# Kernel tuning notes

Measured on AMD Instinct MI355X. Metric: run time of the kernel, lower is better.

Reference implementation:

```python
import jax, jax.numpy as jnp
import numpy as np

B, T, C, H = 4, 4096, 1024, 128

def setup_inputs() -> dict:
    key = jax.random.key(0)
    k1, k2, k3, k4 = jax.random.split(key, 4)
    ix = jax.random.normal(k1, (B, T, C), dtype=jnp.float32)
    Wq = jax.random.normal(k2, (C, H), dtype=jnp.float32) * (C ** -0.5)
    Wk = jax.random.normal(k3, (C, H), dtype=jnp.float32) * (C ** -0.5)
    Wv = jax.random.normal(k4, (C, H), dtype=jnp.float32) * (C ** -0.5)
    return {"ix": ix, "Wq": Wq, "Wk": Wk, "Wv": Wv}

def reference(ix, Wq, Wk, Wv):
    Bc, Tc, Cc = ix.shape
    q = ix @ Wq                      # [B,T,H]
    k = ix @ Wk                      # [B,T,H]
    v = ix @ Wv                      # [B,T,H]
    # NOTE: original computes k @ q^T (row index from k, col index from q),
    # scaled by n_embed**-0.5 (C, not head_size).
    wei = jnp.einsum('bth,bsh->bts', k, q) * (Cc ** -0.5)  # [B,T,T]
    causal = jnp.tril(jnp.ones((Tc, Tc), dtype=bool))
    wei = jnp.where(causal[None, :, :], wei, -jnp.inf)
    wei = jax.nn.softmax(wei, axis=-1)
    # dropout is identity in eval mode
    out = jnp.einsum('bts,bsh->bth', wei, v)  # [B,T,H]
    return out
```

## Files before the change

kernel.cpp:

```cpp
#include <hip/hip_runtime.h>
#include <hip/hip_bf16.h>

typedef __bf16 bf16x8 __attribute__((ext_vector_type(8)));
typedef float f32x4 __attribute__((ext_vector_type(4)));
#define MFMA16 __builtin_amdgcn_mfma_f32_16x16x32_bf16

static constexpr int Bsz = 4, T = 4096, C = 1024, H = 128;
static constexpr int BT = Bsz * T;

__device__ __forceinline__ void gl2lds16(const __bf16* g, __bf16* l) {
    __builtin_amdgcn_global_load_lds(
        (const __attribute__((address_space(1))) void*)g,
        (__attribute__((address_space(3))) void*)l, 16, 0, 0);
}

__global__ __launch_bounds__(256) void k_wprep(
    const float* __restrict__ Wq, const float* __restrict__ Wk,
    const float* __restrict__ Wv, __bf16* __restrict__ WTall)
{
    int idx = blockIdx.x * 256 + threadIdx.x;
    int n = idx >> 10, k = idx & 1023;
    int mat = n >> 7, col = n & 127;
    const float* W = mat == 0 ? Wq : (mat == 1 ? Wk : Wv);
    float s = (mat == 1) ? 0.045084220f : 1.0f;
    WTall[idx] = (__bf16)(W[k * H + col] * s);
}

__global__ __launch_bounds__(512) void k_proj(
    const float* __restrict__ X, const __bf16* __restrict__ WTall,
    __bf16* __restrict__ Qp, __bf16* __restrict__ Kp, __bf16* __restrict__ VT)
{
    union Smem {
        struct { __bf16 a[2][64 * 64]; __bf16 b[2][192 * 64]; } s;
        __bf16 vt_e[128][72];
    };
    __shared__ Smem su;

    const int tid = threadIdx.x;
    const int lane = tid & 63, w = tid >> 6;
    const int c = lane & 15, hi = lane >> 4;
    const int wm = w >> 2, wn = w & 3;
    const int ny = blockIdx.x & 1;
    const int m0 = (blockIdx.x >> 1) * 64;
    const int xorv = (c & 7) << 3;

    const int arow = tid >> 3, ac8 = tid & 7;
    const float* aSrc = X + (size_t)(m0 + arow) * C + ac8 * 8;
    const int aDst = arow * 64 + ((ac8 * 8) ^ ((arow & 7) << 3));
    const int brl = lane >> 3, bch = lane & 7;
    const __bf16* Wbase = WTall + (size_t)ny * 192 * 1024;

    f32x4 acc[2][3];
    #pragma unroll
    for (int i = 0; i < 2; ++i)
        #pragma unroll
        for (int j = 0; j < 3; ++j) acc[i][j] = (f32x4){0.f, 0.f, 0.f, 0.f};

    #pragma unroll
    for (int ib = 0; ib < 3; ++ib) {
        int row = w * 24 + ib * 8 + brl;
        int ch = bch ^ (row & 7);
        gl2lds16(Wbase + (size_t)row * 1024 + ch * 8, &su.s.b[0][(w * 3 + ib) * 512]);
    }
    {
        float4 f0 = *(const float4*)aSrc;
        float4 f1 = *(const float4*)(aSrc + 4);
        bf16x8 av;
        av[0] = (__bf16)f0.x; av[1] = (__bf16)f0.y; av[2] = (__bf16)f0.z; av[3] = (__bf16)f0.w;
        av[4] = (__bf16)f1.x; av[5] = (__bf16)f1.y; av[6] = (__bf16)f1.z; av[7] = (__bf16)f1.w;
        *(bf16x8*)&su.s.a[0][aDst] = av;
    }
    __syncthreads();

    for (int t = 0; t < 16; ++t) {
        int cur = t & 1;
        float4 g0, g1;
        if (t < 15) {
            int k0 = (t + 1) * 64;
            #pragma unroll
            for (int ib = 0; ib < 3; ++ib) {
                int row = w * 24 + ib * 8 + brl;
                int ch = bch ^ (row & 7);
                gl2lds16(Wbase + (size_t)row * 1024 + k0 + ch * 8,
                         &su.s.b[cur ^ 1][(w * 3 + ib) * 512]);
            }
            g0 = *(const float4*)(aSrc + k0);
            g1 = *(const float4*)(aSrc + k0 + 4);
        }
        #pragma unroll
        for (int kk = 0; kk < 2; ++kk) {
            bf16x8 a0 = *(const bf16x8*)&su.s.a[cur][(wm * 32 + c) * 64 + ((kk * 32 + hi * 8) ^ xorv)];
            bf16x8 a1 = *(const bf16x8*)&su.s.a[cur][(wm * 32 + 16 + c) * 64 + ((kk * 32 + hi * 8) ^ xorv)];
            #pragma unroll
            for (int fn = 0; fn < 3; ++fn) {
                bf16x8 bb = *(const bf16x8*)&su.s.b[cur][(wn * 48 + fn * 16 + c) * 64 + ((kk * 32 + hi * 8) ^ xorv)];
                acc[0][fn] = MFMA16(a0, bb, acc[0][fn], 0, 0, 0);
                acc[1][fn] = MFMA16(a1, bb, acc[1][fn], 0, 0, 0);
            }
        }
        if (t < 15) {
            bf16x8 av;
            av[0] = (__bf16)g0.x; av[1] = (__bf16)g0.y; av[2] = (__bf16)g0.z; av[3] = (__bf16)g0.w;
            av[4] = (__bf16)g1.x; av[5] = (__bf16)g1.y; av[6] = (__bf16)g1.z; av[7] = (__bf16)g1.w;
            *(bf16x8*)&su.s.a[cur ^ 1][aDst] = av;
        }
        __syncthreads();
    }

    #pragma unroll
    for (int mi = 0; mi < 2; ++mi) {
        int rowl = wm * 32 + mi * 16 + hi * 4;
        #pragma unroll
        for (int fn = 0; fn < 3; ++fn) {
            int nb = ny * 192 + wn * 48 + fn * 16;
            int mat = nb >> 7, colb = (nb & 127) + c;
            #pragma unroll
            for (int r = 0; r < 4; ++r) {
                __bf16 v = (__bf16)acc[mi][fn][r];
                if (mat == 0)      Qp[(size_t)(m0 + rowl + r) * H + colb] = v;
                else if (mat == 1) Kp[(size_t)(m0 + rowl + r) * H + colb] = v;
                else               su.vt_e[colb][rowl + r] = v;
            }
        }
    }
    __syncthreads();
    if (ny == 1) {
        int d = tid >> 2, tc = (tid & 3) * 16;
        int b = m0 >> 12, tl = m0 & (T - 1);
        __bf16* dst = VT + ((size_t)b * H + d) * T + tl + tc;
        const __bf16* s2 = &su.vt_e[d][tc];
        *(uint4*)dst = *(const uint4*)s2;
        *(uint4*)(dst + 8) = *(const uint4*)(s2 + 8);
    }
}

__global__ __launch_bounds__(256) void k_attn(
    const __bf16* __restrict__ Ka, const __bf16* __restrict__ Qb,
    const __bf16* __restrict__ VT, float* __restrict__ Out,
    float* __restrict__ Po, float* __restrict__ Pl)
{
    __shared__ __bf16 pl[4][32][40];
    __shared__ float oacc[64][132];
    __shared__ float sml[4][32];

    const int tid = threadIdx.x, lane = tid & 63, w = tid >> 6;
    const int c = lane & 15, hi = lane >> 4;
    const int wm = w >> 1, ws = w & 1;

    const int bi = blockIdx.x;
    const int p = bi & 1, b = (bi >> 1) & 3, u = bi >> 3;

    const __bf16* Kb  = Ka + (size_t)b * T * H;
    const __bf16* Qbb = Qb + (size_t)b * T * H;
    const __bf16* Vb  = VT + (size_t)b * H * T;

    bf16x8 ones;
    #pragma unroll
    for (int q8 = 0; q8 < 8; ++q8) ones[q8] = (__bf16)1.0f;

    #pragma unroll 1
    for (int half = 0; half < 2; ++half) {
        const int j  = half ? (63 - u) : u;
        const int t0 = j * 64;
        const int nsteps = j + 1;
        const int rbase = t0 + wm * 32;

        bf16x8 af[2][4];
        #pragma unroll
        for (int mi = 0; mi < 2; ++mi)
            #pragma unroll
            for (int kc = 0; kc < 4; ++kc)
                af[mi][kc] = *(const bf16x8*)(Kb + (size_t)(rbase + mi * 16 + c) * H + kc * 32 + hi * 8);

        f32x4 o[2][8], ol[2];
        #pragma unroll
        for (int mi = 0; mi < 2; ++mi) {
            #pragma unroll
            for (int nt = 0; nt < 8; ++nt) o[mi][nt] = (f32x4){0.f, 0.f, 0.f, 0.f};
            ol[mi] = (f32x4){0.f, 0.f, 0.f, 0.f};
        }

        for (int i = p; i < nsteps; i += 2) {
            const int sbase = i * 64 + ws * 32;
            f32x4 sa[2][2];
            sa[0][0] = (f32x4){0.f, 0.f, 0.f, 0.f}; sa[0][1] = sa[0][0];
            sa[1][0] = sa[0][0]; sa[1][1] = sa[0][0];
            #pragma unroll
            for (int sc = 0; sc < 2; ++sc) {
                bf16x8 bq[4];
                #pragma unroll
                for (int kc = 0; kc < 4; ++kc)
                    bq[kc] = *(const bf16x8*)(Qbb + (size_t)(sbase + sc * 16 + c) * H + kc * 32 + hi * 8);
                #pragma unroll
                for (int kc = 0; kc < 4; ++kc) {
                    sa[0][sc] = MFMA16(af[0][kc], bq[kc], sa[0][sc], 0, 0, 0);
                    sa[1][sc] = MFMA16(af[1][kc], bq[kc], sa[1][sc], 0, 0, 0);
                }
            }
            const bool dz = (sbase + 31 > rbase);
            #pragma unroll
            for (int mi = 0; mi < 2; ++mi)
                #pragma unroll
                for (int sc = 0; sc < 2; ++sc)
                    #pragma unroll
                    for (int r = 0; r < 4; ++r) {
                        float e = __builtin_amdgcn_exp2f(sa[mi][sc][r]);
                        if (dz) {
                            int tg = rbase + mi * 16 + hi * 4 + r;
                            if (sbase + sc * 16 + c > tg) e = 0.f;
                        }
                        pl[w][mi * 16 + hi * 4 + r][sc * 16 + c] = (__bf16)e;
                    }
            #pragma unroll
            for (int mi = 0; mi < 2; ++mi) {
                bf16x8 pf = *(const bf16x8*)&pl[w][mi * 16 + c][hi * 8];
                ol[mi] = MFMA16(pf, ones, ol[mi], 0, 0, 0);
                #pragma unroll
                for (int nt = 0; nt < 8; ++nt) {
                    bf16x8 vb = *(const bf16x8*)(Vb + (size_t)(nt * 16 + c) * T + sbase + hi * 8);
                    o[mi][nt] = MFMA16(pf, vb, o[mi][nt], 0, 0, 0);
                }
            }
        }

        if (c == 0) {
            #pragma unroll
            for (int mi = 0; mi < 2; ++mi)
                #pragma unroll
                for (int r = 0; r < 4; ++r)
                    sml[w][mi * 16 + hi * 4 + r] = ol[mi][r];
        }
        if (ws == 0) {
            #pragma unroll
            for (int mi = 0; mi < 2; ++mi)
                #pragma unroll
                for (int nt = 0; nt < 8; ++nt)
                    #pragma unroll
                    for (int r = 0; r < 4; ++r)
                        oacc[wm * 32 + mi * 16 + hi * 4 + r][nt * 16 + c] = o[mi][nt][r];
        }
        __syncthreads();
        if (ws == 1) {
            #pragma unroll
            for (int mi = 0; mi < 2; ++mi)
                #pragma unroll
                for (int nt = 0; nt < 8; ++nt)
                    #pragma unroll
                    for (int r = 0; r < 4; ++r)
                        oacc[wm * 32 + mi * 16 + hi * 4 + r][nt * 16 + c] += o[mi][nt][r];
        }
        __syncthreads();
        {
            int row = tid >> 2, cq = (tid & 3) * 4;
            float L = sml[(row >> 5) * 2][row & 31] + sml[(row >> 5) * 2 + 1][row & 31];
            float* dst = (p == 0 ? Out : Po) + ((size_t)b * T + t0 + row) * H;
            #pragma unroll
            for (int k = 0; k < 8; ++k) {
                int col = cq + k * 16;
                float4 v;
                v.x = oacc[row][col];
                v.y = oacc[row][col + 1];
                v.z = oacc[row][col + 2];
                v.w = oacc[row][col + 3];
                *(float4*)(dst + col) = v;
            }
            if ((tid & 3) == 0) Pl[(size_t)p * BT + b * T + t0 + row] = L;
        }
        __syncthreads();
    }
}

__global__ __launch_bounds__(256) void k_merge(
    float* __restrict__ Out, const float* __restrict__ Po,
    const float* __restrict__ Pl)
{
    size_t idx = ((size_t)blockIdx.x * 256 + threadIdx.x) * 8;
    size_t row = idx >> 7;
    float inv = 1.0f / (Pl[row] + Pl[BT + row]);
    float4 a0 = *(const float4*)(Out + idx);
    float4 a1 = *(const float4*)(Out + idx + 4);
    float4 p0 = *(const float4*)(Po + idx);
    float4 p1 = *(const float4*)(Po + idx + 4);
    float4 r0, r1;
    r0.x = (a0.x + p0.x) * inv; r0.y = (a0.y + p0.y) * inv;
    r0.z = (a0.z + p0.z) * inv; r0.w = (a0.w + p0.w) * inv;
    r1.x = (a1.x + p1.x) * inv; r1.y = (a1.y + p1.y) * inv;
    r1.z = (a1.z + p1.z) * inv; r1.w = (a1.w + p1.w) * inv;
    *(float4*)(Out + idx)     = r0;
    *(float4*)(Out + idx + 4) = r1;
}

extern "C" void kernel_launch(void* const* d_in, const int* in_sizes, int n_in,
                              void* d_out, int out_size, void* d_ws, size_t ws_size,
                              hipStream_t stream) {
    const float* ix = (const float*)d_in[0];
    const float* Wq = (const float*)d_in[1];
    const float* Wk = (const float*)d_in[2];
    const float* Wv = (const float*)d_in[3];
    float* out = (float*)d_out;

    __bf16* WTall = (__bf16*)d_ws;
    __bf16* Qp = WTall + 393216;
    __bf16* Kp = Qp + (size_t)BT * H;
    __bf16* VT = Kp + (size_t)BT * H;
    float*  Po = (float*)(VT + (size_t)BT * H);
    float*  Pl = Po + (size_t)BT * H;

    k_wprep<<<dim3(1536), 256, 0, stream>>>(Wq, Wk, Wv, WTall);
    k_proj<<<dim3(512), 512, 0, stream>>>(ix, WTall, Qp, Kp, VT);
    k_attn<<<dim3(256), 256, 0, stream>>>(Kp, Qp, VT, out, Po, Pl);
    k_merge<<<dim3(1024), 256, 0, stream>>>(out, Po, Pl);
}
```

Measured before the change: 110.3 us.

## Split attention key loop across 16 waves per block with LDS reduction

The attention kernel grows from 4 to 16 waves per block. The extra waves split the causal key steps four ways inside each block, and their partial output and row-sum accumulators are combined in shared memory over 8 serialized passes separated by barriers. The goal is to raise occupancy and latency hiding, since each CU previously ran only 4 waves. The P·V inner loop is also reordered so each V fragment is loaded once and reused for both row tiles. The cost is extra reduction passes and barriers, plus a 1024-thread launch bound that caps per-wave registers and may cause spills.

```diff
diff --git a/kernel.cpp b/kernel.cpp
--- a/kernel.cpp
+++ b/kernel.cpp
@@ -134,18 +134,18 @@
     }
 }
 
-__global__ __launch_bounds__(256) void k_attn(
+__global__ __launch_bounds__(1024) void k_attn(
     const __bf16* __restrict__ Ka, const __bf16* __restrict__ Qb,
     const __bf16* __restrict__ VT, float* __restrict__ Out,
     float* __restrict__ Po, float* __restrict__ Pl)
 {
-    __shared__ __bf16 pl[4][32][40];
+    __shared__ __bf16 pl[16][32][40];
     __shared__ float oacc[64][132];
-    __shared__ float sml[4][32];
+    __shared__ float sml[16][32];
 
     const int tid = threadIdx.x, lane = tid & 63, w = tid >> 6;
     const int c = lane & 15, hi = lane >> 4;
-    const int wm = w >> 1, ws = w & 1;
+    const int wm = (w >> 3) & 1, ws = (w >> 2) & 1, sp = w & 3;
 
     const int bi = blockIdx.x;
     const int p = bi & 1, b = (bi >> 1) & 3, u = bi >> 3;
@@ -180,7 +180,7 @@
             ol[mi] = (f32x4){0.f, 0.f, 0.f, 0.f};
         }
 
-        for (int i = p; i < nsteps; i += 2) {
+        for (int i = p + 2 * sp; i < nsteps; i += 8) {
             const int sbase = i * 64 + ws * 32;
             f32x4 sa[2][2];
             sa[0][0] = (f32x4){0.f, 0.f, 0.f, 0.f}; sa[0][1] = sa[0][0];
@@ -211,15 +211,15 @@
                         }
                         pl[w][mi * 16 + hi * 4 + r][sc * 16 + c] = (__bf16)e;
                     }
-            #pragma unroll
-            for (int mi = 0; mi < 2; ++mi) {
-                bf16x8 pf = *(const bf16x8*)&pl[w][mi * 16 + c][hi * 8];
-                ol[mi] = MFMA16(pf, ones, ol[mi], 0, 0, 0);
-                #pragma unroll
-                for (int nt = 0; nt < 8; ++nt) {
-                    bf16x8 vb = *(const bf16x8*)(Vb + (size_t)(nt * 16 + c) * T + sbase + hi * 8);
-                    o[mi][nt] = MFMA16(pf, vb, o[mi][nt], 0, 0, 0);
-                }
+            bf16x8 pf0 = *(const bf16x8*)&pl[w][c][hi * 8];
+            bf16x8 pf1 = *(const bf16x8*)&pl[w][16 + c][hi * 8];
+            ol[0] = MFMA16(pf0, ones, ol[0], 0, 0, 0);
+            ol[1] = MFMA16(pf1, ones, ol[1], 0, 0, 0);
+            #pragma unroll
+            for (int nt = 0; nt < 8; ++nt) {
+                bf16x8 vb = *(const bf16x8*)(Vb + (size_t)(nt * 16 + c) * T + sbase + hi * 8);
+                o[0][nt] = MFMA16(pf0, vb, o[0][nt], 0, 0, 0);
+                o[1][nt] = MFMA16(pf1, vb, o[1][nt], 0, 0, 0);
             }
         }
 
@@ -230,41 +230,36 @@
                 for (int r = 0; r < 4; ++r)
                     sml[w][mi * 16 + hi * 4 + r] = ol[mi][r];
         }
-        if (ws == 0) {
-            #pragma unroll
-            for (int mi = 0; mi < 2; ++mi)
-                #pragma unroll
-                for (int nt = 0; nt < 8; ++nt)
+        __syncthreads();
+        for (int g = 0; g < 8; ++g) {
+            if ((w & 7) == g) {
+                #pragma unroll
+                for (int mi = 0; mi < 2; ++mi)
                     #pragma unroll
-                    for (int r = 0; r < 4; ++r)
-                        oacc[wm * 32 + mi * 16 + hi * 4 + r][nt * 16 + c] = o[mi][nt][r];
-        }
-        __syncthreads();
-        if (ws == 1) {
-            #pragma unroll
-            for (int mi = 0; mi < 2; ++mi)
-                #pragma unroll
-                for (int nt = 0; nt < 8; ++nt)
-                    #pragma unroll
-                    for (int r = 0; r < 4; ++r)
-                        oacc[wm * 32 + mi * 16 + hi * 4 + r][nt * 16 + c] += o[mi][nt][r];
-        }
-        __syncthreads();
+                    for (int nt = 0; nt < 8; ++nt)
+                        #pragma unroll
+                        for (int r = 0; r < 4; ++r) {
+                            int row = wm * 32 + mi * 16 + hi * 4 + r, col = nt * 16 + c;
+                            if (g == 0) oacc[row][col]  = o[mi][nt][r];
+                            else        oacc[row][col] += o[mi][nt][r];
+                        }
+            }
+            __syncthreads();
+        }
         {
-            int row = tid >> 2, cq = (tid & 3) * 4;
-            float L = sml[(row >> 5) * 2][row & 31] + sml[(row >> 5) * 2 + 1][row & 31];
-            float* dst = (p == 0 ? Out : Po) + ((size_t)b * T + t0 + row) * H;
-            #pragma unroll
-            for (int k = 0; k < 8; ++k) {
-                int col = cq + k * 16;
-                float4 v;
-                v.x = oacc[row][col];
-                v.y = oacc[row][col + 1];
-                v.z = oacc[row][col + 2];
-                v.w = oacc[row][col + 3];
-                *(float4*)(dst + col) = v;
-            }
-            if ((tid & 3) == 0) Pl[(size_t)p * BT + b * T + t0 + row] = L;
+            int row = tid >> 4, col0 = (tid & 15) * 8;
+            float L = 0.f;
+            #pragma unroll
+            for (int g = 0; g < 8; ++g) L += sml[(row >> 5) * 8 + g][row & 31];
+            float* dst = (p == 0 ? Out : Po) + ((size_t)b * T + t0 + row) * H + col0;
+            float4 v0, v1;
+            v0.x = oacc[row][col0];     v0.y = oacc[row][col0 + 1];
+            v0.z = oacc[row][col0 + 2]; v0.w = oacc[row][col0 + 3];
+            v1.x = oacc[row][col0 + 4]; v1.y = oacc[row][col0 + 5];
+            v1.z = oacc[row][col0 + 6]; v1.w = oacc[row][col0 + 7];
+            *(float4*)dst       = v0;
+            *(float4*)(dst + 4) = v1;
+            if ((tid & 15) == 0) Pl[(size_t)p * BT + b * T + t0 + row] = L;
         }
         __syncthreads();
     }
@@ -308,6 +303,6 @@
 
     k_wprep<<<dim3(1536), 256, 0, stream>>>(Wq, Wk, Wv, WTall);
     k_proj<<<dim3(512), 512, 0, stream>>>(ix, WTall, Qp, Kp, VT);
-    k_attn<<<dim3(256), 256, 0, stream>>>(Kp, Qp, VT, out, Po, Pl);
+    k_attn<<<dim3(256), 1024, 0, stream>>>(Kp, Qp, VT, out, Po, Pl);
     k_merge<<<dim3(1024), 256, 0, stream>>>(out, Po, Pl);
 }
```

Measured after the change: 155.5 us. 1.41x slower.

## Software-pipeline Q/V register loads in attention loop and remap projection block indices

Applied to the files above, without the earlier changes.

The attention inner loop now double-buffers the Q and V fragments in registers, issuing global loads for the next step before computing the current one so memory latency overlaps the MFMA and exp work. The MFMAs are also interleaved across independent accumulators. Separately, the projection kernel's block index mapping changes so consecutive blocks cover different row tiles of the same weight half instead of alternating halves. Keeping a second set of fragments live raises register pressure and can reduce occupancy. The diagonal mask condition also changes from > to >=, which is harmless.

```diff
diff --git a/kernel.cpp b/kernel.cpp
--- a/kernel.cpp
+++ b/kernel.cpp
@@ -40,8 +40,8 @@
     const int lane = tid & 63, w = tid >> 6;
     const int c = lane & 15, hi = lane >> 4;
     const int wm = w >> 2, wn = w & 3;
-    const int ny = blockIdx.x & 1;
-    const int m0 = (blockIdx.x >> 1) * 64;
+    const int ny = blockIdx.x >> 8;
+    const int m0 = (blockIdx.x & 255) * 64;
     const int xorv = (c & 7) << 3;
 
     const int arow = tid >> 3, ac8 = tid & 7;
@@ -180,48 +180,71 @@
             ol[mi] = (f32x4){0.f, 0.f, 0.f, 0.f};
         }
 
-        for (int i = p; i < nsteps; i += 2) {
-            const int sbase = i * 64 + ws * 32;
-            f32x4 sa[2][2];
-            sa[0][0] = (f32x4){0.f, 0.f, 0.f, 0.f}; sa[0][1] = sa[0][0];
-            sa[1][0] = sa[0][0]; sa[1][1] = sa[0][0];
-            #pragma unroll
-            for (int sc = 0; sc < 2; ++sc) {
-                bf16x8 bq[4];
-                #pragma unroll
-                for (int kc = 0; kc < 4; ++kc)
-                    bq[kc] = *(const bf16x8*)(Qbb + (size_t)(sbase + sc * 16 + c) * H + kc * 32 + hi * 8);
-                #pragma unroll
-                for (int kc = 0; kc < 4; ++kc) {
-                    sa[0][sc] = MFMA16(af[0][kc], bq[kc], sa[0][sc], 0, 0, 0);
-                    sa[1][sc] = MFMA16(af[1][kc], bq[kc], sa[1][sc], 0, 0, 0);
-                }
-            }
-            const bool dz = (sbase + 31 > rbase);
-            #pragma unroll
-            for (int mi = 0; mi < 2; ++mi)
-                #pragma unroll
-                for (int sc = 0; sc < 2; ++sc)
-                    #pragma unroll
-                    for (int r = 0; r < 4; ++r) {
-                        float e = __builtin_amdgcn_exp2f(sa[mi][sc][r]);
-                        if (dz) {
-                            int tg = rbase + mi * 16 + hi * 4 + r;
-                            if (sbase + sc * 16 + c > tg) e = 0.f;
-                        }
-                        pl[w][mi * 16 + hi * 4 + r][sc * 16 + c] = (__bf16)e;
-                    }
-            #pragma unroll
-            for (int mi = 0; mi < 2; ++mi) {
-                bf16x8 pf = *(const bf16x8*)&pl[w][mi * 16 + c][hi * 8];
-                ol[mi] = MFMA16(pf, ones, ol[mi], 0, 0, 0);
-                #pragma unroll
-                for (int nt = 0; nt < 8; ++nt) {
-                    bf16x8 vb = *(const bf16x8*)(Vb + (size_t)(nt * 16 + c) * T + sbase + hi * 8);
-                    o[mi][nt] = MFMA16(pf, vb, o[mi][nt], 0, 0, 0);
-                }
-            }
-        }
+        bf16x8 bqA[8], vbA[8], bqB[8], vbB[8];
+
+#define LOADSTEP(BQ, VB, I) {                                                    \
+            const int sb_ = (I) * 64 + ws * 32;                                  \
+            _Pragma("unroll")                                                    \
+            for (int sc = 0; sc < 2; ++sc)                                       \
+                _Pragma("unroll")                                                \
+                for (int kc = 0; kc < 4; ++kc)                                   \
+                    BQ[sc * 4 + kc] = *(const bf16x8*)(Qbb +                     \
+                        (size_t)(sb_ + sc * 16 + c) * H + kc * 32 + hi * 8);     \
+            _Pragma("unroll")                                                    \
+            for (int nt = 0; nt < 8; ++nt)                                       \
+                VB[nt] = *(const bf16x8*)(Vb + (size_t)(nt * 16 + c) * T + sb_ + hi * 8); }
+
+#define COMPSTEP(BQ, VB, I) {                                                    \
+            const int sb_ = (I) * 64 + ws * 32;                                  \
+            f32x4 sa[2][2];                                                      \
+            sa[0][0] = (f32x4){0.f,0.f,0.f,0.f}; sa[0][1] = sa[0][0];            \
+            sa[1][0] = sa[0][0]; sa[1][1] = sa[0][0];                            \
+            _Pragma("unroll")                                                    \
+            for (int kc = 0; kc < 4; ++kc) {                                     \
+                sa[0][0] = MFMA16(af[0][kc], BQ[kc],     sa[0][0], 0, 0, 0);     \
+                sa[0][1] = MFMA16(af[0][kc], BQ[4 + kc], sa[0][1], 0, 0, 0);     \
+                sa[1][0] = MFMA16(af[1][kc], BQ[kc],     sa[1][0], 0, 0, 0);     \
+                sa[1][1] = MFMA16(af[1][kc], BQ[4 + kc], sa[1][1], 0, 0, 0);     \
+            }                                                                    \
+            const bool dz = (sb_ + 31 >= rbase);                                 \
+            _Pragma("unroll")                                                    \
+            for (int mi = 0; mi < 2; ++mi)                                       \
+                _Pragma("unroll")                                                \
+                for (int sc = 0; sc < 2; ++sc)                                   \
+                    _Pragma("unroll")                                            \
+                    for (int r = 0; r < 4; ++r) {                                \
+                        float e = __builtin_amdgcn_exp2f(sa[mi][sc][r]);         \
+                        if (dz) {                                                \
+                            int tg = rbase + mi * 16 + hi * 4 + r;               \
+                            if (sb_ + sc * 16 + c > tg) e = 0.f;                 \
+                        }                                                        \
+                        pl[w][mi * 16 + hi * 4 + r][sc * 16 + c] = (__bf16)e;    \
+                    }                                                            \
+            bf16x8 pf0 = *(const bf16x8*)&pl[w][c][hi * 8];                      \
+            bf16x8 pf1 = *(const bf16x8*)&pl[w][16 + c][hi * 8];                 \
+            ol[0] = MFMA16(pf0, ones, ol[0], 0, 0, 0);                           \
+            ol[1] = MFMA16(pf1, ones, ol[1], 0, 0, 0);                           \
+            _Pragma("unroll")                                                    \
+            for (int nt = 0; nt < 8; ++nt) {                                     \
+                o[0][nt] = MFMA16(pf0, VB[nt], o[0][nt], 0, 0, 0);               \
+                o[1][nt] = MFMA16(pf1, VB[nt], o[1][nt], 0, 0, 0);               \
+            } }
+
+        int i = p;
+        if (i < nsteps) LOADSTEP(bqA, vbA, i);
+        while (i < nsteps) {
+            int i2 = i + 2;
+            if (i2 < nsteps) LOADSTEP(bqB, vbB, i2);
+            COMPSTEP(bqA, vbA, i);
+            i = i2;
+            if (i >= nsteps) break;
+            i2 = i + 2;
+            if (i2 < nsteps) LOADSTEP(bqA, vbA, i2);
+            COMPSTEP(bqB, vbB, i);
+            i = i2;
+        }
+#undef LOADSTEP
+#undef COMPSTEP
 
         if (c == 0) {
             #pragma unroll
```

New measurement: 107.9 us. 1.02x faster.

## Switch attention to 32x32 MFMA with register-resident P via lane shuffles

Applied to the files above, without the earlier changes.

Rewrites the attention inner loop to use 32x32x16 bf16 MFMA instead of 16x16x32, computing the score tile transposed (Q as A operand) so each lane holds its K row's probabilities. The softmax probabilities are packed to bf16 and exchanged between half-waves with shuffles, so P never goes through LDS, and the row sum is a scalar add instead of an MFMA against a ones vector. The projection kernel's block-to-tile mapping also changes so the two column halves are split across the grid halves rather than interleaved. This raises register pressure from 32x32 accumulators and larger operand arrays, and relies on the MFMA output layout being mapped correctly.

```diff
diff --git a/kernel.cpp b/kernel.cpp
--- a/kernel.cpp
+++ b/kernel.cpp
@@ -3,7 +3,10 @@
 
 typedef __bf16 bf16x8 __attribute__((ext_vector_type(8)));
 typedef float f32x4 __attribute__((ext_vector_type(4)));
+typedef float f32x16 __attribute__((ext_vector_type(16)));
+typedef unsigned u32x4 __attribute__((ext_vector_type(4)));
 #define MFMA16 __builtin_amdgcn_mfma_f32_16x16x32_bf16
+#define MFMA32 __builtin_amdgcn_mfma_f32_32x32x16_bf16
 
 static constexpr int Bsz = 4, T = 4096, C = 1024, H = 128;
 static constexpr int BT = Bsz * T;
@@ -12,6 +15,12 @@
     __builtin_amdgcn_global_load_lds(
         (const __attribute__((address_space(1))) void*)g,
         (__attribute__((address_space(3))) void*)l, 16, 0, 0);
+}
+
+__device__ __forceinline__ unsigned pk2(float a, float b) {
+    unsigned short ua = __builtin_bit_cast(unsigned short, (__bf16)a);
+    unsigned short ub = __builtin_bit_cast(unsigned short, (__bf16)b);
+    return (unsigned)ua | ((unsigned)ub << 16);
 }
 
 __global__ __launch_bounds__(256) void k_wprep(
@@ -40,8 +49,8 @@
     const int lane = tid & 63, w = tid >> 6;
     const int c = lane & 15, hi = lane >> 4;
     const int wm = w >> 2, wn = w & 3;
-    const int ny = blockIdx.x & 1;
-    const int m0 = (blockIdx.x >> 1) * 64;
+    const int ny = blockIdx.x >> 8;
+    const int m0 = (blockIdx.x & 255) * 64;
     const int xorv = (c & 7) << 3;
 
     const int arow = tid >> 3, ac8 = tid & 7;
@@ -139,12 +148,11 @@
     const __bf16* __restrict__ VT, float* __restrict__ Out,
     float* __restrict__ Po, float* __restrict__ Pl)
 {
-    __shared__ __bf16 pl[4][32][40];
     __shared__ float oacc[64][132];
     __shared__ float sml[4][32];
 
     const int tid = threadIdx.x, lane = tid & 63, w = tid >> 6;
-    const int c = lane & 15, hi = lane >> 4;
+    const int t31 = lane & 31, hi5 = lane >> 5;
     const int wm = w >> 1, ws = w & 1;
 
     const int bi = blockIdx.x;
@@ -153,10 +161,6 @@
     const __bf16* Kb  = Ka + (size_t)b * T * H;
     const __bf16* Qbb = Qb + (size_t)b * T * H;
     const __bf16* Vb  = VT + (size_t)b * H * T;
-
-    bf16x8 ones;
-    #pragma unroll
-    for (int q8 = 0; q8 < 8; ++q8) ones[q8] = (__bf16)1.0f;
 
     #pragma unroll 1
     for (int half = 0; half < 2; ++half) {
@@ -164,90 +168,100 @@
         const int t0 = j * 64;
         const int nsteps = j + 1;
         const int rbase = t0 + wm * 32;
-
-        bf16x8 af[2][4];
-        #pragma unroll
-        for (int mi = 0; mi < 2; ++mi)
-            #pragma unroll
-            for (int kc = 0; kc < 4; ++kc)
-                af[mi][kc] = *(const bf16x8*)(Kb + (size_t)(rbase + mi * 16 + c) * H + kc * 32 + hi * 8);
-
-        f32x4 o[2][8], ol[2];
-        #pragma unroll
-        for (int mi = 0; mi < 2; ++mi) {
-            #pragma unroll
-            for (int nt = 0; nt < 8; ++nt) o[mi][nt] = (f32x4){0.f, 0.f, 0.f, 0.f};
-            ol[mi] = (f32x4){0.f, 0.f, 0.f, 0.f};
-        }
+        const int tg = rbase + t31;
+
+        bf16x8 kb[8];
+        #pragma unroll
+        for (int kc = 0; kc < 8; ++kc)
+            kb[kc] = *(const bf16x8*)(Kb + (size_t)(rbase + t31) * H + kc * 16 + hi5 * 8);
+
+        f32x16 oc[4];
+        #pragma unroll
+        for (int dn = 0; dn < 4; ++dn)
+            #pragma unroll
+            for (int r = 0; r < 16; ++r) oc[dn][r] = 0.f;
+        float ol = 0.f;
 
         for (int i = p; i < nsteps; i += 2) {
             const int sbase = i * 64 + ws * 32;
-            f32x4 sa[2][2];
-            sa[0][0] = (f32x4){0.f, 0.f, 0.f, 0.f}; sa[0][1] = sa[0][0];
-            sa[1][0] = sa[0][0]; sa[1][1] = sa[0][0];
-            #pragma unroll
-            for (int sc = 0; sc < 2; ++sc) {
-                bf16x8 bq[4];
+            bf16x8 qa[8];
+            #pragma unroll
+            for (int kc = 0; kc < 8; ++kc)
+                qa[kc] = *(const bf16x8*)(Qbb + (size_t)(sbase + t31) * H + kc * 16 + hi5 * 8);
+            bf16x8 vb[4][2];
+            #pragma unroll
+            for (int dn = 0; dn < 4; ++dn)
                 #pragma unroll
-                for (int kc = 0; kc < 4; ++kc)
-                    bq[kc] = *(const bf16x8*)(Qbb + (size_t)(sbase + sc * 16 + c) * H + kc * 32 + hi * 8);
+                for (int ks = 0; ks < 2; ++ks)
+                    vb[dn][ks] = *(const bf16x8*)(Vb + (size_t)(dn * 32 + t31) * T + sbase + ks * 16 + hi5 * 8);
+
+            f32x16 accA, accB;
+            #pragma unroll
+            for (int r = 0; r < 16; ++r) { accA[r] = 0.f; accB[r] = 0.f; }
+            #pragma unroll
+            for (int kc = 0; kc < 4; ++kc) accA = MFMA32(qa[kc], kb[kc], accA, 0, 0, 0);
+            #pragma unroll
+            for (int kc = 4; kc < 8; ++kc) accB = MFMA32(qa[kc], kb[kc], accB, 0, 0, 0);
+
+            const bool dz = (sbase + 31 >= rbase);
+            float pv[16];
+            #pragma unroll
+            for (int r = 0; r < 16; ++r) {
+                float e = __builtin_amdgcn_exp2f(accA[r] + accB[r]);
+                if (dz) {
+                    int sg = sbase + (r & 3) + 8 * (r >> 2) + 4 * hi5;
+                    if (sg > tg) e = 0.f;
+                }
+                pv[r] = e;
+            }
+            float rs = ((pv[0] + pv[1]) + (pv[2] + pv[3])) + ((pv[4] + pv[5]) + (pv[6] + pv[7]))
+                     + ((pv[8] + pv[9]) + (pv[10] + pv[11])) + ((pv[12] + pv[13]) + (pv[14] + pv[15]));
+            ol += rs;
+
+            unsigned x1 = pk2(pv[0], pv[1]),  x2 = pk2(pv[2], pv[3]);
+            unsigned y1 = pk2(pv[4], pv[5]),  y2 = pk2(pv[6], pv[7]);
+            unsigned x3 = pk2(pv[8], pv[9]),  x4 = pk2(pv[10], pv[11]);
+            unsigned y3 = pk2(pv[12], pv[13]), y4 = pk2(pv[14], pv[15]);
+            unsigned sx1 = __shfl_xor((int)x1, 32), sx2 = __shfl_xor((int)x2, 32);
+            unsigned sy1 = __shfl_xor((int)y1, 32), sy2 = __shfl_xor((int)y2, 32);
+            unsigned sx3 = __shfl_xor((int)x3, 32), sx4 = __shfl_xor((int)x4, 32);
+            unsigned sy3 = __shfl_xor((int)y3, 32), sy4 = __shfl_xor((int)y4, 32);
+            u32x4 wA, wB;
+            wA[0] = hi5 ? sy1 : x1;  wA[1] = hi5 ? sy2 : x2;
+            wA[2] = hi5 ? y1 : sx1;  wA[3] = hi5 ? y2 : sx2;
+            wB[0] = hi5 ? sy3 : x3;  wB[1] = hi5 ? sy4 : x4;
+            wB[2] = hi5 ? y3 : sx3;  wB[3] = hi5 ? y4 : sx4;
+            bf16x8 paA = __builtin_bit_cast(bf16x8, wA);
+            bf16x8 paB = __builtin_bit_cast(bf16x8, wB);
+
+            #pragma unroll
+            for (int dn = 0; dn < 4; ++dn) {
+                oc[dn] = MFMA32(paA, vb[dn][0], oc[dn], 0, 0, 0);
+                oc[dn] = MFMA32(paB, vb[dn][1], oc[dn], 0, 0, 0);
+            }
+        }
+
+        ol += __shfl_xor(ol, 32);
+        if (lane < 32) sml[w][lane] = ol;
+
+        if (ws == 0) {
+            #pragma unroll
+            for (int dn = 0; dn < 4; ++dn)
                 #pragma unroll
-                for (int kc = 0; kc < 4; ++kc) {
-                    sa[0][sc] = MFMA16(af[0][kc], bq[kc], sa[0][sc], 0, 0, 0);
-                    sa[1][sc] = MFMA16(af[1][kc], bq[kc], sa[1][sc], 0, 0, 0);
+                for (int r = 0; r < 16; ++r) {
+                    int row = wm * 32 + (r & 3) + 8 * (r >> 2) + 4 * hi5;
+                    oacc[row][dn * 32 + t31] = oc[dn][r];
                 }
-            }
-            const bool dz = (sbase + 31 > rbase);
-            #pragma unroll
-            for (int mi = 0; mi < 2; ++mi)
-                #pragma unroll
-                for (int sc = 0; sc < 2; ++sc)
-                    #pragma unroll
-                    for (int r = 0; r < 4; ++r) {
-                        float e = __builtin_amdgcn_exp2f(sa[mi][sc][r]);
-                        if (dz) {
-                            int tg = rbase + mi * 16 + hi * 4 + r;
-                            if (sbase + sc * 16 + c > tg) e = 0.f;
-                        }
-                        pl[w][mi * 16 + hi * 4 + r][sc * 16 + c] = (__bf16)e;
-                    }
-            #pragma unroll
-            for (int mi = 0; mi < 2; ++mi) {
-                bf16x8 pf = *(const bf16x8*)&pl[w][mi * 16 + c][hi * 8];
-                ol[mi] = MFMA16(pf, ones, ol[mi], 0, 0, 0);
-                #pragma unroll
-                for (int nt = 0; nt < 8; ++nt) {
-                    bf16x8 vb = *(const bf16x8*)(Vb + (size_t)(nt * 16 + c) * T + sbase + hi * 8);
-                    o[mi][nt] = MFMA16(pf, vb, o[mi][nt], 0, 0, 0);
-                }
-            }
-        }
-
-        if (c == 0) {
-            #pragma unroll
-            for (int mi = 0; mi < 2; ++mi)
-                #pragma unroll
-                for (int r = 0; r < 4; ++r)
-                    sml[w][mi * 16 + hi * 4 + r] = ol[mi][r];
-        }
-        if (ws == 0) {
-            #pragma unroll
-            for (int mi = 0; mi < 2; ++mi)
-                #pragma unroll
-                for (int nt = 0; nt < 8; ++nt)
-                    #pragma unroll
-                    for (int r = 0; r < 4; ++r)
-                        oacc[wm * 32 + mi * 16 + hi * 4 + r][nt * 16 + c] = o[mi][nt][r];
         }
         __syncthreads();
         if (ws == 1) {
             #pragma unroll
-            for (int mi = 0; mi < 2; ++mi)
+            for (int dn = 0; dn < 4; ++dn)
                 #pragma unroll
-                for (int nt = 0; nt < 8; ++nt)
-                    #pragma unroll
-                    for (int r = 0; r < 4; ++r)
-                        oacc[wm * 32 + mi * 16 + hi * 4 + r][nt * 16 + c] += o[mi][nt][r];
+                for (int r = 0; r < 16; ++r) {
+                    int row = wm * 32 + (r & 3) + 8 * (r >> 2) + 4 * hi5;
+                    oacc[row][dn * 32 + t31] += oc[dn][r];
+                }
         }
         __syncthreads();
         {
```

New measurement: 106.7 us. 3.2% less time.
